# Kernel optimization log

Hardware: AMD Instinct MI355X
Metric: run time of the kernel (lower is better)

The kernel has to match this reference:

```python
import jax, jax.numpy as jnp
import numpy as np

D_MODEL = 1024
NUM_HEADS = 16
D_K = D_MODEL // NUM_HEADS
SCALE = D_K ** 0.5


def setup_inputs() -> dict:
    key = jax.random.key(0)
    ks = jax.random.split(key, 11)
    B, S = 2, 2048
    std = 1.0 / np.sqrt(D_MODEL)
    inp = {
        "query": jax.random.normal(ks[0], (B, S, D_MODEL), dtype=jnp.float32),
        "key": jax.random.normal(ks[1], (B, S, D_MODEL), dtype=jnp.float32),
        "value": jax.random.normal(ks[2], (B, S, D_MODEL), dtype=jnp.float32),
        "wq": jax.random.uniform(ks[3], (D_MODEL, D_MODEL), jnp.float32, -std, std),
        "bq": jax.random.uniform(ks[4], (D_MODEL,), jnp.float32, -std, std),
        "wk": jax.random.uniform(ks[5], (D_MODEL, D_MODEL), jnp.float32, -std, std),
        "bk": jax.random.uniform(ks[6], (D_MODEL,), jnp.float32, -std, std),
        "wv": jax.random.uniform(ks[7], (D_MODEL, D_MODEL), jnp.float32, -std, std),
        "bv": jax.random.uniform(ks[8], (D_MODEL,), jnp.float32, -std, std),
        "wo": jax.random.uniform(ks[9], (D_MODEL, D_MODEL), jnp.float32, -std, std),
        "bo": jax.random.uniform(ks[10], (D_MODEL,), jnp.float32, -std, std),
    }
    return inp


def _split_heads(x):
    # [B, S, d_model] -> [B, H, S, d_k]
    B, S, _ = x.shape
    return x.reshape(B, S, NUM_HEADS, D_K).transpose(0, 2, 1, 3)


def reference(query, key, value, wq, bq, wk, bk, wv, bv, wo, bo):
    # Linear layers: torch Linear computes x @ W^T + b; weights here stored as [out, in]
    q = _split_heads(query @ wq.T + bq)  # [B, H, S, d_k]
    k = _split_heads(key @ wk.T + bk)
    v = _split_heads(value @ wv.T + bv)
    scores = jnp.einsum("bhqd,bhkd->bhqk", q, k) / SCALE  # [B, H, Sq, Sk]
    attn = jax.nn.softmax(scores, axis=-1)
    ctx = jnp.einsum("bhqk,bhkd->bhqd", attn, v)  # [B, H, S, d_k]
    B, H, S, dk = ctx.shape
    ctx = ctx.transpose(0, 2, 1, 3).reshape(B, S, D_MODEL)
    return ctx @ wo.T + bo
```

## Files before the change

### kernel.cpp

```cpp
#include <hip/hip_runtime.h>
#include <hip/hip_bf16.h>


typedef __attribute__((ext_vector_type(8))) short short8;
typedef __attribute__((ext_vector_type(4))) float floatx4;

#define D_MODEL 1024
#define SEQ 2048
#define NTOK 4096
#define DK 64
#define NH 16
#define MAT 4194304
#define WMAT 1048576

static __device__ __forceinline__ unsigned short f2bf(float f) {
    unsigned int x = __float_as_uint(f);
    unsigned int r = x + 0x7fffu + ((x >> 16) & 1u);
    return (unsigned short)(r >> 16);
}
static __device__ __forceinline__ float bf2f(unsigned short u) {
    return __uint_as_float(((unsigned int)u) << 16);
}
static __device__ __forceinline__ unsigned pk2(float x, float y) {
    __hip_bfloat162 h = __float22bfloat162_rn(make_float2(x, y));
    return *reinterpret_cast<unsigned*>(&h);
}
static __device__ __forceinline__ short8 cvt8(float4 f0, float4 f1) {
    union { unsigned u[4]; short8 s; } r;
    r.u[0] = pk2(f0.x, f0.y); r.u[1] = pk2(f0.z, f0.w);
    r.u[2] = pk2(f1.x, f1.y); r.u[3] = pk2(f1.z, f1.w);
    return r.s;
}
static __device__ __forceinline__ int permtok(int t) {
    return ((t >> 2) & 3) * 16 + ((t >> 4) & 3) * 4 + (t & 3);
}
static __device__ __forceinline__ void glds16(const unsigned short* g, unsigned short* l) {
    __builtin_amdgcn_global_load_lds(
        (const __attribute__((address_space(1))) void*)g,
        (__attribute__((address_space(3))) void*)l, 16, 0, 0);
}

__global__ __launch_bounds__(256) void cvt7(
    const float* __restrict__ s0, const float* __restrict__ s1,
    const float* __restrict__ s2, const float* __restrict__ s3,
    const float* __restrict__ s4, const float* __restrict__ s5,
    const float* __restrict__ s6, unsigned short* __restrict__ dst) {
    const float* s; size_t doff; int n;
    switch (blockIdx.y) {
        case 0: s = s0; doff = 0;                          n = MAT;  break;
        case 1: s = s1; doff = (size_t)MAT;                n = MAT;  break;
        case 2: s = s2; doff = (size_t)2 * MAT;            n = MAT;  break;
        case 3: s = s3; doff = (size_t)3 * MAT;            n = WMAT; break;
        case 4: s = s4; doff = (size_t)3 * MAT + WMAT;     n = WMAT; break;
        case 5: s = s5; doff = (size_t)3 * MAT + 2 * WMAT; n = WMAT; break;
        default: s = s6; doff = (size_t)3 * MAT + 3 * WMAT; n = WMAT; break;
    }
    int idx = (blockIdx.x * 256 + threadIdx.x) * 8;
    if (idx >= n) return;
    float4 a = *(const float4*)(s + idx);
    float4 b = *(const float4*)(s + idx + 4);
    *(short8*)&dst[doff + idx] = cvt8(a, b);
}

template <bool F32OUT, int BM>
static __device__ __forceinline__ void gemm_bb(const unsigned short* __restrict__ X,
                                               const unsigned short* __restrict__ W,
                                               const float* __restrict__ bias,
                                               void* __restrict__ outp,
                                               int m0, int n0,
                                               int ostride, bool rowbias, bool permn) {
    __shared__ __align__(16) unsigned short Asm[BM * 64];
    __shared__ __align__(16) unsigned short Bsm[128 * 64];
    constexpr int MF = BM / 32;
    constexpr int HALF = BM / 2;

    const int tid = threadIdx.x;
    const int lane = tid & 63;
    const int wv = tid >> 6;
    const int g = lane >> 4;
    const int lm = lane & 15;
    const int wr = wv >> 1;
    const int wc = wv & 1;
    const int rs = (lm & 7) << 3;
    const int lr = lane >> 3;
    const int lc = lane & 7;

    auto issue = [&](int k0) {
#pragma unroll
        for (int i = 0; i < BM / 32; ++i) {
            const int r0 = wv * (BM / 4) + i * 8;
            const int row = r0 + lr;
            const int gcol = (lc ^ (row & 7)) << 3;
            glds16(&X[(size_t)(m0 + row) * 1024 + k0 + gcol], &Asm[r0 * 64]);
        }
#pragma unroll
        for (int i = 0; i < 4; ++i) {
            const int r0 = wv * 32 + i * 8;
            const int row = r0 + lr;
            const int gcol = (lc ^ (row & 7)) << 3;
            glds16(&W[(size_t)(n0 + row) * 1024 + k0 + gcol], &Bsm[r0 * 64]);
        }
    };

    floatx4 acc[MF][4];
#pragma unroll
    for (int mi = 0; mi < MF; ++mi)
#pragma unroll
        for (int ni = 0; ni < 4; ++ni)
            acc[mi][ni] = (floatx4){0.f, 0.f, 0.f, 0.f};

    issue(0);
    for (int k0 = 0; k0 < 1024; k0 += 64) {
        __syncthreads();
#pragma unroll
        for (int ks = 0; ks < 64; ks += 32) {
            short8 af[MF], bfr[4];
#pragma unroll
            for (int mi = 0; mi < MF; ++mi)
                af[mi] = *(const short8*)&Asm[(wr * HALF + mi * 16 + lm) * 64 +
                                              ((ks + g * 8) ^ rs)];
#pragma unroll
            for (int ni = 0; ni < 4; ++ni)
                bfr[ni] = *(const short8*)&Bsm[(wc * 64 + ni * 16 + lm) * 64 +
                                               ((ks + g * 8) ^ rs)];
#pragma unroll
            for (int mi = 0; mi < MF; ++mi)
#pragma unroll
                for (int ni = 0; ni < 4; ++ni)
                    acc[mi][ni] = __builtin_amdgcn_mfma_f32_16x16x32_bf16(
                        af[mi], bfr[ni], acc[mi][ni], 0, 0, 0);
        }
        __syncthreads();
        if (k0 + 64 < 1024) issue(k0 + 64);
    }

    float cb[4];
#pragma unroll
    for (int ni = 0; ni < 4; ++ni)
        cb[ni] = rowbias ? 0.f : bias[n0 + wc * 64 + ni * 16 + lm];
#pragma unroll
    for (int mi = 0; mi < MF; ++mi)
#pragma unroll
        for (int r = 0; r < 4; ++r) {
            int rowg = m0 + wr * HALF + mi * 16 + g * 4 + r;
            float rb = rowbias ? bias[rowg] : 0.f;
#pragma unroll
            for (int ni = 0; ni < 4; ++ni) {
                int colg = n0 + wc * 64 + ni * 16 + lm;
                if (permn) colg = (colg & ~63) | permtok(colg & 63);
                float val = acc[mi][ni][r] + (rowbias ? rb : cb[ni]);
                if (F32OUT)
                    ((float*)outp)[(size_t)rowg * ostride + colg] = val;
                else
                    ((unsigned short*)outp)[(size_t)rowg * ostride + colg] = f2bf(val);
            }
        }
}

__global__ __launch_bounds__(256) void proj_gemm_b(
    const unsigned short* __restrict__ Xb, const unsigned short* __restrict__ Wb,
    const float* __restrict__ bq, const float* __restrict__ bk,
    const float* __restrict__ bv, unsigned short* __restrict__ QK,
    unsigned short* __restrict__ VT) {
    const int z = blockIdx.z;
    const int bid = blockIdx.x;
    if (z == 0)
        gemm_bb<false, 128>(Xb, Wb, bq, QK,
                            (bid >> 3) * 128, (bid & 7) * 128, 1024, false, false);
    else if (z == 1)
        gemm_bb<false, 128>(Xb + (size_t)MAT, Wb + (size_t)WMAT, bk,
                            QK + (size_t)MAT,
                            (bid >> 3) * 128, (bid & 7) * 128, 1024, false, false);
    else
        gemm_bb<false, 128>(Wb + (size_t)2 * WMAT, Xb + (size_t)2 * MAT, bv, VT,
                            (bid & 7) * 128, (bid >> 3) * 128, 4096, true, true);
}

__global__ __launch_bounds__(256) void out_gemm_b(
    const unsigned short* __restrict__ ctx, const unsigned short* __restrict__ Wo,
    const float* __restrict__ bo, float* __restrict__ out) {
    gemm_bb<true, 64>(ctx, Wo, bo, out, blockIdx.y * 64, blockIdx.x * 128,
                      1024, false, false);
}

template <bool ROWBIAS, bool PERMN, int OSTRIDE>
static __device__ __forceinline__ void gemm128_f(const float* __restrict__ X,
                                                 const float* __restrict__ W,
                                                 const float* __restrict__ bias,
                                                 unsigned short* __restrict__ out) {
    __shared__ __align__(16) unsigned short Asm[128 * 72];
    __shared__ __align__(16) unsigned short Bsm[128 * 72];
    const int tid = threadIdx.x;
    const int lane = tid & 63;
    const int wv = tid >> 6;
    const int g = lane >> 4;
    const int lm = lane & 15;
    const int wr = wv >> 1;
    const int wc = wv & 1;
    const int m0 = blockIdx.y * 128;
    const int n0 = blockIdx.x * 128;
    floatx4 acc[4][4];
#pragma unroll
    for (int mi = 0; mi < 4; ++mi)
#pragma unroll
        for (int ni = 0; ni < 4; ++ni)
            acc[mi][ni] = (floatx4){0.f, 0.f, 0.f, 0.f};
    for (int k0 = 0; k0 < 1024; k0 += 64) {
#pragma unroll
        for (int i = 0; i < 4; ++i) {
            int idx = tid + i * 256;
            int row = idx >> 3;
            int col = (idx & 7) << 3;
            const float* sa = &X[(size_t)(m0 + row) * 1024 + k0 + col];
            *(short8*)&Asm[row * 72 + col] = cvt8(*(const float4*)sa, *(const float4*)(sa + 4));
            const float* sb = &W[(size_t)(n0 + row) * 1024 + k0 + col];
            *(short8*)&Bsm[row * 72 + col] = cvt8(*(const float4*)sb, *(const float4*)(sb + 4));
        }
        __syncthreads();
#pragma unroll
        for (int ks = 0; ks < 64; ks += 32) {
            short8 af[4], bfr[4];
#pragma unroll
            for (int mi = 0; mi < 4; ++mi)
                af[mi] = *(const short8*)&Asm[(wr * 64 + mi * 16 + lm) * 72 + ks + g * 8];
#pragma unroll
            for (int ni = 0; ni < 4; ++ni)
                bfr[ni] = *(const short8*)&Bsm[(wc * 64 + ni * 16 + lm) * 72 + ks + g * 8];
#pragma unroll
            for (int mi = 0; mi < 4; ++mi)
#pragma unroll
                for (int ni = 0; ni < 4; ++ni)
                    acc[mi][ni] = __builtin_amdgcn_mfma_f32_16x16x32_bf16(
                        af[mi], bfr[ni], acc[mi][ni], 0, 0, 0);
        }
        __syncthreads();
    }
    float cb[4];
#pragma unroll
    for (int ni = 0; ni < 4; ++ni)
        cb[ni] = ROWBIAS ? 0.f : bias[n0 + wc * 64 + ni * 16 + lm];
#pragma unroll
    for (int mi = 0; mi < 4; ++mi)
#pragma unroll
        for (int r = 0; r < 4; ++r) {
            int rowg = m0 + wr * 64 + mi * 16 + g * 4 + r;
            float rb = ROWBIAS ? bias[rowg] : 0.f;
#pragma unroll
            for (int ni = 0; ni < 4; ++ni) {
                int colg = n0 + wc * 64 + ni * 16 + lm;
                if (PERMN) colg = (colg & ~63) | permtok(colg & 63);
                out[(size_t)rowg * OSTRIDE + colg] =
                    f2bf(acc[mi][ni][r] + (ROWBIAS ? rb : cb[ni]));
            }
        }
}

__global__ __launch_bounds__(256) void qkv_gemm_f(
    const float* __restrict__ xq, const float* __restrict__ xk,
    const float* __restrict__ wq, const float* __restrict__ wk,
    const float* __restrict__ bq, const float* __restrict__ bk,
    unsigned short* __restrict__ q, unsigned short* __restrict__ k) {
    if (blockIdx.z == 0) gemm128_f<false, false, 1024>(xq, wq, bq, q);
    else                 gemm128_f<false, false, 1024>(xk, wk, bk, k);
}

__global__ __launch_bounds__(256) void vt_gemm_f(
    const float* __restrict__ wv, const float* __restrict__ xv,
    const float* __restrict__ bv, unsigned short* __restrict__ VT) {
    gemm128_f<true, true, 4096>(wv, xv, bv, VT);
}

__global__ __launch_bounds__(256) void out_gemm_f(
    const float* __restrict__ wo, const float* __restrict__ bo,
    const unsigned short* __restrict__ ctx, float* __restrict__ out) {
    __shared__ __align__(16) unsigned short Asm[128 * 72];
    __shared__ __align__(16) unsigned short Bsm[128 * 72];
    const int tid = threadIdx.x;
    const int lane = tid & 63;
    const int wv = tid >> 6;
    const int g = lane >> 4;
    const int lm = lane & 15;
    const int wr = wv >> 1;
    const int wc = wv & 1;
    const int m0 = blockIdx.y * 128;
    const int n0 = blockIdx.x * 128;
    floatx4 acc[4][4];
#pragma unroll
    for (int mi = 0; mi < 4; ++mi)
#pragma unroll
        for (int ni = 0; ni < 4; ++ni)
            acc[mi][ni] = (floatx4){0.f, 0.f, 0.f, 0.f};
    for (int k0 = 0; k0 < 1024; k0 += 64) {
#pragma unroll
        for (int i = 0; i < 4; ++i) {
            int idx = tid + i * 256;
            int row = idx >> 3;
            int col = (idx & 7) << 3;
            *(uint4*)&Asm[row * 72 + col] =
                *(const uint4*)&ctx[(size_t)(m0 + row) * 1024 + k0 + col];
            const float* sb = &wo[(size_t)(n0 + row) * 1024 + k0 + col];
            *(short8*)&Bsm[row * 72 + col] = cvt8(*(const float4*)sb, *(const float4*)(sb + 4));
        }
        __syncthreads();
#pragma unroll
        for (int ks = 0; ks < 64; ks += 32) {
            short8 af[4], bfr[4];
#pragma unroll
            for (int mi = 0; mi < 4; ++mi)
                af[mi] = *(const short8*)&Asm[(wr * 64 + mi * 16 + lm) * 72 + ks + g * 8];
#pragma unroll
            for (int ni = 0; ni < 4; ++ni)
                bfr[ni] = *(const short8*)&Bsm[(wc * 64 + ni * 16 + lm) * 72 + ks + g * 8];
#pragma unroll
            for (int mi = 0; mi < 4; ++mi)
#pragma unroll
                for (int ni = 0; ni < 4; ++ni)
                    acc[mi][ni] = __builtin_amdgcn_mfma_f32_16x16x32_bf16(
                        af[mi], bfr[ni], acc[mi][ni], 0, 0, 0);
        }
        __syncthreads();
    }
    float bb[4];
#pragma unroll
    for (int ni = 0; ni < 4; ++ni)
        bb[ni] = bo[n0 + wc * 64 + ni * 16 + lm];
#pragma unroll
    for (int mi = 0; mi < 4; ++mi)
#pragma unroll
        for (int ni = 0; ni < 4; ++ni)
#pragma unroll
            for (int r = 0; r < 4; ++r) {
                int rowg = m0 + wr * 64 + mi * 16 + g * 4 + r;
                int colg = n0 + wc * 64 + ni * 16 + lm;
                out[(size_t)rowg * 1024 + colg] = acc[mi][ni][r] + bb[ni];
            }
}

__global__ __launch_bounds__(256) void attn_kernel(
    const unsigned short* __restrict__ Q, const unsigned short* __restrict__ K,
    const unsigned short* __restrict__ VT, unsigned short* __restrict__ CTX) {
    __shared__ __align__(16) unsigned short Ksm[2][128 * 64];
    __shared__ __align__(16) unsigned short Vtsm[2][128 * 64];

    const int tid = threadIdx.x;
    const int lane = tid & 63;
    const int w = tid >> 6;
    const int g = lane >> 4;
    const int lm = lane & 15;
    const int bh = blockIdx.x;
    const int qt = blockIdx.y;
    const int b = bh >> 4;
    const int h = bh & 15;

    const size_t base = (size_t)b * SEQ * D_MODEL + (size_t)h * DK;
    const size_t vtbase = (size_t)(h * 64) * NTOK + (size_t)b * SEQ;
    const int rs = (lm & 7) << 3;
    const int lr = lane >> 3;
    const int lc = lane & 7;

    union { unsigned u[4]; short8 s; } onev;
    onev.u[0] = 0x3F803F80u; onev.u[1] = 0x3F803F80u;
    onev.u[2] = 0x3F803F80u; onev.u[3] = 0x3F803F80u;

    short8 qf[2][2];
#pragma unroll
    for (int qs = 0; qs < 2; ++qs) {
        const int qrow = qt * 128 + w * 32 + qs * 16 + lm;
#pragma unroll
        for (int t = 0; t < 2; ++t) {
            short8 raw = *(const short8*)&Q[base + (size_t)qrow * D_MODEL + t * 32 + g * 8];
            union { unsigned u[4]; short8 s; } r;
#pragma unroll
            for (int j = 0; j < 4; ++j) {
                float lo = bf2f((unsigned short)raw[2 * j]) * 0.1803368801f;
                float hi = bf2f((unsigned short)raw[2 * j + 1]) * 0.1803368801f;
                r.u[j] = pk2(lo, hi);
            }
            qf[qs][t] = r.s;
        }
    }

    floatx4 Oacc[2][4];
    floatx4 Lacc[2];
#pragma unroll
    for (int qs = 0; qs < 2; ++qs) {
        Lacc[qs] = (floatx4){0.f, 0.f, 0.f, 0.f};
#pragma unroll
        for (int nb = 0; nb < 4; ++nb) Oacc[qs][nb] = (floatx4){0.f, 0.f, 0.f, 0.f};
    }

    auto issue_pair = [&](int pr, int p) {
        const int krow0 = pr * 128;
#pragma unroll
        for (int i = 0; i < 4; ++i) {
            const int r0 = w * 32 + i * 8;
            const int row = r0 + lr;
            const int gcol = (lc ^ (row & 7)) << 3;
            glds16(&K[base + (size_t)(krow0 + row) * D_MODEL + gcol], &Ksm[p][r0 * 64]);
            glds16(&VT[vtbase + (size_t)(row & 63) * NTOK + krow0 + (row >> 6) * 64 + gcol],
                   &Vtsm[p][r0 * 64]);
        }
    };

    const int NP = SEQ / 128;
    issue_pair(0, 0);
    issue_pair(1, 1);
    for (int pr = 0; pr < NP; ++pr) {
        const int p = pr & 1;
        if (pr + 1 < NP) asm volatile("s_waitcnt vmcnt(8)" ::: "memory");
        else             asm volatile("s_waitcnt vmcnt(0)" ::: "memory");
        __builtin_amdgcn_s_barrier();

#pragma unroll
        for (int s = 0; s < 2; ++s) {
            const unsigned short* Kt = &Ksm[p][s * 4096];
            const unsigned short* Vv = &Vtsm[p][s * 4096];

            float pa[2][4][4];
#pragma unroll
            for (int kb = 0; kb < 4; ++kb) {
                short8 ak0 = *(const short8*)&Kt[(kb * 16 + lm) * 64 + ((0 + g * 8) ^ rs)];
                short8 ak1 = *(const short8*)&Kt[(kb * 16 + lm) * 64 + ((32 + g * 8) ^ rs)];
#pragma unroll
                for (int qs = 0; qs < 2; ++qs) {
                    floatx4 a = (floatx4){0.f, 0.f, 0.f, 0.f};
                    __builtin_amdgcn_s_setprio(1);
                    a = __builtin_amdgcn_mfma_f32_16x16x32_bf16(ak0, qf[qs][0], a, 0, 0, 0);
                    a = __builtin_amdgcn_mfma_f32_16x16x32_bf16(ak1, qf[qs][1], a, 0, 0, 0);
                    __builtin_amdgcn_s_setprio(0);
#pragma unroll
                    for (int r = 0; r < 4; ++r) pa[qs][kb][r] = __builtin_amdgcn_exp2f(a[r]);
                }
            }

#pragma unroll
            for (int cp = 0; cp < 2; ++cp) {
                const int c0 = 2 * cp, c1 = 2 * cp + 1;
                union { unsigned u[4]; short8 s; } ap[2];
#pragma unroll
                for (int qs = 0; qs < 2; ++qs) {
                    ap[qs].u[0] = pk2(pa[qs][c0][0], pa[qs][c0][1]);
                    ap[qs].u[1] = pk2(pa[qs][c0][2], pa[qs][c0][3]);
                    ap[qs].u[2] = pk2(pa[qs][c1][0], pa[qs][c1][1]);
                    ap[qs].u[3] = pk2(pa[qs][c1][2], pa[qs][c1][3]);
                }
                __builtin_amdgcn_s_setprio(1);
#pragma unroll
                for (int nb = 0; nb < 4; ++nb) {
                    const int d = nb * 16 + lm;
                    short8 bv = *(const short8*)&Vv[d * 64 + ((g * 16 + cp * 8) ^ rs)];
                    Oacc[0][nb] = __builtin_amdgcn_mfma_f32_16x16x32_bf16(
                        ap[0].s, bv, Oacc[0][nb], 0, 0, 0);
                    Oacc[1][nb] = __builtin_amdgcn_mfma_f32_16x16x32_bf16(
                        ap[1].s, bv, Oacc[1][nb], 0, 0, 0);
                }
                Lacc[0] = __builtin_amdgcn_mfma_f32_16x16x32_bf16(
                    ap[0].s, onev.s, Lacc[0], 0, 0, 0);
                Lacc[1] = __builtin_amdgcn_mfma_f32_16x16x32_bf16(
                    ap[1].s, onev.s, Lacc[1], 0, 0, 0);
                __builtin_amdgcn_s_setprio(0);
            }
        }

        __builtin_amdgcn_s_barrier();
        if (pr + 2 < NP) issue_pair(pr + 2, p);
    }

#pragma unroll
    for (int qs = 0; qs < 2; ++qs) {
        float rl[4];
#pragma unroll
        for (int r = 0; r < 4; ++r) rl[r] = 1.0f / Lacc[qs][r];
#pragma unroll
        for (int nb = 0; nb < 4; ++nb) {
#pragma unroll
            for (int r = 0; r < 4; ++r) {
                float val = Oacc[qs][nb][r] * rl[r];
                int srow = qt * 128 + w * 32 + qs * 16 + g * 4 + r;
                CTX[base + (size_t)srow * D_MODEL + nb * 16 + lm] = f2bf(val);
            }
        }
    }
}

extern "C" void kernel_launch(void* const* d_in, const int* in_sizes, int n_in,
                              void* d_out, int out_size, void* d_ws, size_t ws_size,
                              hipStream_t stream) {
    const float* xq = (const float*)d_in[0];
    const float* xk = (const float*)d_in[1];
    const float* xv = (const float*)d_in[2];
    const float* wq = (const float*)d_in[3];
    const float* bq = (const float*)d_in[4];
    const float* wk = (const float*)d_in[5];
    const float* bk = (const float*)d_in[6];
    const float* wv = (const float*)d_in[7];
    const float* bv = (const float*)d_in[8];
    const float* wo = (const float*)d_in[9];
    const float* bo = (const float*)d_in[10];
    float* out = (float*)d_out;

    unsigned short* ws = (unsigned short*)d_ws;

    if (ws_size >= (size_t)68 * 1024 * 1024) {
        unsigned short* Xb = ws;
        unsigned short* Wb = ws + (size_t)3 * MAT;
        unsigned short* Qw = Wb + (size_t)4 * WMAT;
        unsigned short* Kw = Qw + (size_t)MAT;
        unsigned short* VTw = Kw + (size_t)MAT;
        unsigned short* Cw = VTw + (size_t)MAT;

        cvt7<<<dim3(2048, 7), 256, 0, stream>>>(xq, xk, xv, wq, wk, wv, wo, ws);
        proj_gemm_b<<<dim3(256, 1, 3), 256, 0, stream>>>(Xb, Wb, bq, bk, bv, Qw, VTw);
        attn_kernel<<<dim3(2 * NH, SEQ / 128), 256, 0, stream>>>(Qw, Kw, VTw, Cw);
        out_gemm_b<<<dim3(8, 64), 256, 0, stream>>>(Cw, Wb + (size_t)3 * WMAT, bo, out);
    } else {
        unsigned short* Qw = ws;
        unsigned short* Kw = ws + (size_t)MAT;
        unsigned short* VTw = ws + (size_t)2 * MAT;
        unsigned short* Cw = ws + (size_t)3 * MAT;
        qkv_gemm_f<<<dim3(8, 32, 2), 256, 0, stream>>>(xq, xk, wq, wk, bq, bk, Qw, Kw);
        vt_gemm_f<<<dim3(32, 8), 256, 0, stream>>>(wv, xv, bv, VTw);
        attn_kernel<<<dim3(2 * NH, SEQ / 128), 256, 0, stream>>>(Qw, Kw, VTw, Cw);
        out_gemm_f<<<dim3(8, 32), 256, 0, stream>>>(wo, bo, Cw, out);
    }
}
```

Baseline: 224.8 us.

## Fuse fp32-to-bf16 activation conversion into projection GEMM staging

The separate conversion kernel now only converts the four weight matrices. The projection GEMM reads fp32 activations directly, converts them to bf16 in registers and writes them into swizzled shared memory. This removes a full bf16 write and re-read of the three activation tensors. In exchange, the activation loads become synchronous register loads instead of async global-to-LDS copies, and each GEMM tile re-reads fp32 data from global memory, which costs more bandwidth per tile and risks stalls in the GEMM main loop.

```diff
diff --git a/kernel.cpp b/kernel.cpp
--- a/kernel.cpp
+++ b/kernel.cpp
@@ -40,39 +40,42 @@
         (__attribute__((address_space(3))) void*)l, 16, 0, 0);
 }
 
-__global__ __launch_bounds__(256) void cvt7(
-    const float* __restrict__ s0, const float* __restrict__ s1,
-    const float* __restrict__ s2, const float* __restrict__ s3,
-    const float* __restrict__ s4, const float* __restrict__ s5,
-    const float* __restrict__ s6, unsigned short* __restrict__ dst) {
-    const float* s; size_t doff; int n;
+__global__ __launch_bounds__(256) void cvt4(
+    const float* __restrict__ w0, const float* __restrict__ w1,
+    const float* __restrict__ w2, const float* __restrict__ w3,
+    unsigned short* __restrict__ dst) {
+    const float* s;
     switch (blockIdx.y) {
-        case 0: s = s0; doff = 0;                          n = MAT;  break;
-        case 1: s = s1; doff = (size_t)MAT;                n = MAT;  break;
-        case 2: s = s2; doff = (size_t)2 * MAT;            n = MAT;  break;
-        case 3: s = s3; doff = (size_t)3 * MAT;            n = WMAT; break;
-        case 4: s = s4; doff = (size_t)3 * MAT + WMAT;     n = WMAT; break;
-        case 5: s = s5; doff = (size_t)3 * MAT + 2 * WMAT; n = WMAT; break;
-        default: s = s6; doff = (size_t)3 * MAT + 3 * WMAT; n = WMAT; break;
-    }
+        case 0: s = w0; break;
+        case 1: s = w1; break;
+        case 2: s = w2; break;
+        default: s = w3; break;
+    }
+    size_t doff = (size_t)blockIdx.y * WMAT;
     int idx = (blockIdx.x * 256 + threadIdx.x) * 8;
-    if (idx >= n) return;
     float4 a = *(const float4*)(s + idx);
     float4 b = *(const float4*)(s + idx + 4);
     *(short8*)&dst[doff + idx] = cvt8(a, b);
 }
 
 template <bool F32OUT, int BM>
-static __device__ __forceinline__ void gemm_bb(const unsigned short* __restrict__ X,
-                                               const unsigned short* __restrict__ W,
+static __device__ __forceinline__ void gemm_bb(const void* __restrict__ Xp,
+                                               const void* __restrict__ Wp,
                                                const float* __restrict__ bias,
                                                void* __restrict__ outp,
                                                int m0, int n0,
-                                               int ostride, bool rowbias, bool permn) {
+                                               int ostride, bool rowbias, bool permn,
+                                               bool af32, bool bf32) {
     __shared__ __align__(16) unsigned short Asm[BM * 64];
     __shared__ __align__(16) unsigned short Bsm[128 * 64];
     constexpr int MF = BM / 32;
     constexpr int HALF = BM / 2;
+    constexpr int ACH = BM / 32;
+
+    const unsigned short* Xb = (const unsigned short*)Xp;
+    const float* Xf = (const float*)Xp;
+    const unsigned short* Wbb = (const unsigned short*)Wp;
+    const float* Wf = (const float*)Wp;
 
     const int tid = threadIdx.x;
     const int lane = tid & 63;
@@ -84,21 +87,58 @@
     const int rs = (lm & 7) << 3;
     const int lr = lane >> 3;
     const int lc = lane & 7;
-
-    auto issue = [&](int k0) {
-#pragma unroll
-        for (int i = 0; i < BM / 32; ++i) {
-            const int r0 = wv * (BM / 4) + i * 8;
-            const int row = r0 + lr;
-            const int gcol = (lc ^ (row & 7)) << 3;
-            glds16(&X[(size_t)(m0 + row) * 1024 + k0 + gcol], &Asm[r0 * 64]);
-        }
-#pragma unroll
-        for (int i = 0; i < 4; ++i) {
-            const int r0 = wv * 32 + i * 8;
-            const int row = r0 + lr;
-            const int gcol = (lc ^ (row & 7)) << 3;
-            glds16(&W[(size_t)(n0 + row) * 1024 + k0 + gcol], &Bsm[r0 * 64]);
+    const int srow = tid >> 3;
+    const int scol = (tid & 7) << 3;
+
+    float4 fa[2 * ACH];
+    float4 fb[8];
+
+    auto stage = [&](int k0) {
+        if (af32) {
+#pragma unroll
+            for (int i = 0; i < ACH; ++i) {
+                const int row = srow + i * 32;
+                const float* s = &Xf[(size_t)(m0 + row) * 1024 + k0 + scol];
+                fa[2 * i] = *(const float4*)s;
+                fa[2 * i + 1] = *(const float4*)(s + 4);
+            }
+#pragma unroll
+            for (int i = 0; i < ACH; ++i) {
+                const int row = srow + i * 32;
+                const int sc = scol ^ ((row & 7) << 3);
+                *(short8*)&Asm[row * 64 + sc] = cvt8(fa[2 * i], fa[2 * i + 1]);
+            }
+        } else {
+#pragma unroll
+            for (int i = 0; i < BM / 32; ++i) {
+                const int r0 = wv * (BM / 4) + i * 8;
+                const int row = r0 + lr;
+                const int gcol = (lc ^ (row & 7)) << 3;
+                glds16(&Xb[(size_t)(m0 + row) * 1024 + k0 + gcol], &Asm[r0 * 64]);
+            }
+        }
+        if (bf32) {
+#pragma unroll
+            for (int i = 0; i < 4; ++i) {
+                const int row = srow + i * 32;
+                const float* s = &Wf[(size_t)(n0 + row) * 1024 + k0 + scol];
+                fb[2 * i] = *(const float4*)s;
+                fb[2 * i + 1] = *(const float4*)(s + 4);
+            }
+#pragma unroll
+            for (int i = 0; i < 4; ++i) {
+                const int row = srow + i * 32;
+                const int sc = scol ^ ((row & 7) << 3);
+                *(short8*)&Bsm[row * 64 + sc] = cvt8(fb[2 * i], fb[2 * i + 1]);
+            }
+        } else {
+#pragma unroll
+            for (int i = 0; i < 4; ++i) {
+                const int r0 = wv * 32 + i * 8;
+                const int row = r0 + lr;
+                const int gcol = (lc ^ (row & 7)) << 3;
+                glds16(&Wbb[(size_t)(n0 + row) * 1024 + k0 + gcol], &Bsm[r0 * 64]);
+            }
         }
     };
 
@@ -109,7 +149,7 @@
         for (int ni = 0; ni < 4; ++ni)
             acc[mi][ni] = (floatx4){0.f, 0.f, 0.f, 0.f};
 
-    issue(0);
+    stage(0);
     for (int k0 = 0; k0 < 1024; k0 += 64) {
         __syncthreads();
 #pragma unroll
@@ -131,7 +171,7 @@
                         af[mi], bfr[ni], acc[mi][ni], 0, 0, 0);
         }
         __syncthreads();
-        if (k0 + 64 < 1024) issue(k0 + 64);
+        if (k0 + 64 < 1024) stage(k0 + 64);
     }
 
     float cb[4];
@@ -158,29 +198,32 @@
 }
 
 __global__ __launch_bounds__(256) void proj_gemm_b(
-    const unsigned short* __restrict__ Xb, const unsigned short* __restrict__ Wb,
+    const float* __restrict__ xq, const float* __restrict__ xk,
+    const float* __restrict__ xv, const unsigned short* __restrict__ Wb,
     const float* __restrict__ bq, const float* __restrict__ bk,
     const float* __restrict__ bv, unsigned short* __restrict__ QK,
     unsigned short* __restrict__ VT) {
     const int z = blockIdx.z;
     const int bid = blockIdx.x;
     if (z == 0)
-        gemm_bb<false, 128>(Xb, Wb, bq, QK,
-                            (bid >> 3) * 128, (bid & 7) * 128, 1024, false, false);
+        gemm_bb<false, 128>(xq, Wb, bq, QK,
+                            (bid >> 3) * 128, (bid & 7) * 128, 1024, false, false,
+                            true, false);
     else if (z == 1)
-        gemm_bb<false, 128>(Xb + (size_t)MAT, Wb + (size_t)WMAT, bk,
-                            QK + (size_t)MAT,
-                            (bid >> 3) * 128, (bid & 7) * 128, 1024, false, false);
+        gemm_bb<false, 128>(xk, Wb + (size_t)WMAT, bk, QK + (size_t)MAT,
+                            (bid >> 3) * 128, (bid & 7) * 128, 1024, false, false,
+                            true, false);
     else
-        gemm_bb<false, 128>(Wb + (size_t)2 * WMAT, Xb + (size_t)2 * MAT, bv, VT,
-                            (bid & 7) * 128, (bid >> 3) * 128, 4096, true, true);
+        gemm_bb<false, 128>(Wb + (size_t)2 * WMAT, xv, bv, VT,
+                            (bid & 7) * 128, (bid >> 3) * 128, 4096, true, true,
+                            false, true);
 }
 
 __global__ __launch_bounds__(256) void out_gemm_b(
     const unsigned short* __restrict__ ctx, const unsigned short* __restrict__ Wo,
     const float* __restrict__ bo, float* __restrict__ out) {
     gemm_bb<true, 64>(ctx, Wo, bo, out, blockIdx.y * 64, blockIdx.x * 128,
-                      1024, false, false);
+                      1024, false, false, false, false);
 }
 
 template <bool ROWBIAS, bool PERMN, int OSTRIDE>
@@ -502,15 +545,15 @@
     unsigned short* ws = (unsigned short*)d_ws;
 
     if (ws_size >= (size_t)68 * 1024 * 1024) {
-        unsigned short* Xb = ws;
-        unsigned short* Wb = ws + (size_t)3 * MAT;
+        unsigned short* Wb = ws;
         unsigned short* Qw = Wb + (size_t)4 * WMAT;
         unsigned short* Kw = Qw + (size_t)MAT;
         unsigned short* VTw = Kw + (size_t)MAT;
         unsigned short* Cw = VTw + (size_t)MAT;
 
-        cvt7<<<dim3(2048, 7), 256, 0, stream>>>(xq, xk, xv, wq, wk, wv, wo, ws);
-        proj_gemm_b<<<dim3(256, 1, 3), 256, 0, stream>>>(Xb, Wb, bq, bk, bv, Qw, VTw);
+        cvt4<<<dim3(512, 4), 256, 0, stream>>>(wq, wk, wv, wo, Wb);
+        proj_gemm_b<<<dim3(256, 1, 3), 256, 0, stream>>>(xq, xk, xv, Wb,
+                                                         bq, bk, bv, Qw, VTw);
         attn_kernel<<<dim3(2 * NH, SEQ / 128), 256, 0, stream>>>(Qw, Kw, VTw, Cw);
         out_gemm_b<<<dim3(8, 64), 256, 0, stream>>>(Cw, Wb + (size_t)3 * WMAT, bo, out);
     } else {
```

Result: slower. 241.5 us (+7.4%).
